# Kernel optimization log

Measured on AMD Instinct MI355X. Metric: run time of the kernel, lower is better.

## Reference

```python
import jax, jax.numpy as jnp
import numpy as np

NUM_EMBEDDINGS = 1024
EMBEDDING_DIM = 64
COMMITMENT_COST = 0.25


def setup_inputs() -> dict:
    key = jax.random.key(0)
    k1, k2 = jax.random.split(key)
    inputs = jax.random.normal(k1, (8, 128, 128, EMBEDDING_DIM), dtype=jnp.float32)
    # nn.Embedding init: uniform(-1/K, 1/K)
    codebook = jax.random.uniform(
        k2, (NUM_EMBEDDINGS, EMBEDDING_DIM), dtype=jnp.float32,
        minval=-1.0 / NUM_EMBEDDINGS, maxval=1.0 / NUM_EMBEDDINGS)
    return {"inputs": inputs, "codebook": codebook}


def reference(inputs, codebook):
    input_shape = inputs.shape
    flat = inputs.reshape(-1, EMBEDDING_DIM)  # [N, D]
    distances = (jnp.sum(flat * flat, axis=1, keepdims=True)
                 + jnp.sum(codebook * codebook, axis=1)
                 - 2.0 * jnp.matmul(flat, codebook.T))  # [N, K]
    encoding_indices = jnp.argmin(distances, axis=1)  # [N]
    # one-hot @ codebook == direct gather
    quantized = codebook[encoding_indices].reshape(input_shape)
    e_latent_loss = jnp.mean((jax.lax.stop_gradient(quantized) - inputs) ** 2)
    q_latent_loss = jnp.mean((quantized - jax.lax.stop_gradient(inputs)) ** 2)
    vq_loss = q_latent_loss + COMMITMENT_COST * e_latent_loss
    # straight-through estimator
    quantized = inputs + jax.lax.stop_gradient(quantized - inputs)
    return (quantized, vq_loss, encoding_indices[:, None])
```

## Files before the change

kernel.cpp:

```cpp
#include <hip/hip_runtime.h>


typedef _Float16 f16x8 __attribute__((ext_vector_type(8)));
typedef float f32x4 __attribute__((ext_vector_type(4)));

constexpr int Dm = 64;
constexpr int Kn = 1024;
constexpr long NR = 131072;
constexpr long QE = NR * (long)Dm;
constexpr int RB = 64;
constexpr int NBLK = (int)(NR / RB);
constexpr int CH = 64;
constexpr int NCH = Kn / CH;
constexpr int SP4 = 17;

constexpr size_t SE_OFF   = 0;
constexpr size_t CBH_OFF  = 4096;
constexpr size_t CNT_OFF  = CBH_OFF + 131072;
constexpr size_t HARD_OFF = CNT_OFF + 256;
constexpr size_t PART_OFF = HARD_OFF + 4 * 131072;
constexpr size_t WS_REQ   = PART_OFF + 16384;

__global__ __launch_bounds__(256) void vq_prep(const float* __restrict__ cb,
                                               float* __restrict__ se,
                                               _Float16* __restrict__ cbh,
                                               int* __restrict__ cnt)
{
    int j = blockIdx.x * 256 + threadIdx.x;
    const float* e = cb + (size_t)j * Dm;
    _Float16* h = cbh + (size_t)j * Dm;
    float s = 0.f;
    #pragma unroll
    for (int d = 0; d < Dm; ++d) s = fmaf(e[d], e[d], s);
    se[j] = s;
    #pragma unroll
    for (int d = 0; d < Dm; ++d) h[d] = (_Float16)(e[d] * 1024.0f);
    if (j == 0) *cnt = 0;
}

__global__ __launch_bounds__(256, 4) void vq_pass1(
    const float* __restrict__ inp, const _Float16* __restrict__ cbh,
    const float* __restrict__ seg, float* __restrict__ out,
    int* __restrict__ hard_list, int* __restrict__ cnt)
{
    __shared__ __align__(16) _Float16 xh[RB * 72];
    __shared__ float se[Kn];
    __shared__ float gs[RB];
    __shared__ float wm1[4][RB], wm2[4][RB];
    __shared__ int   wi1[4][RB];

    const int tid = threadIdx.x;
    const long rbase = (long)blockIdx.x * RB;

    #pragma unroll
    for (int k = 0; k < 4; ++k) se[tid + 256 * k] = seg[tid + 256 * k];

    {
        const int r = tid >> 2, q = tid & 3;
        const float* src = inp + (rbase + r) * Dm + q * 16;
        _Float16* dst = xh + r * 72 + q * 16;
        #pragma unroll
        for (int i = 0; i < 4; ++i) {
            float4 v = *reinterpret_cast<const float4*>(src + 4 * i);
            dst[4*i+0] = (_Float16)v.x; dst[4*i+1] = (_Float16)v.y;
            dst[4*i+2] = (_Float16)v.z; dst[4*i+3] = (_Float16)v.w;
        }
    }
    if (tid < RB) {
        const float* xr = inp + (rbase + tid) * Dm;
        float g = 0.f;
        #pragma unroll
        for (int d = 0; d < Dm; ++d) g += fabsf(xr[d]);
        gs[tid] = g;
    }
    __syncthreads();

    const int w = tid >> 6, l = tid & 63;
    const int arow = l & 15, kg = l >> 4;

    f16x8 a0[4], a1[4];
    #pragma unroll
    for (int rt = 0; rt < 4; ++rt) {
        const _Float16* ap = xh + (rt * 16 + arow) * 72 + kg * 8;
        a0[rt] = *reinterpret_cast<const f16x8*>(ap);
        a1[rt] = *reinterpret_cast<const f16x8*>(ap + 32);
    }

    float mn1[4][4], mn2[4][4]; int ix1[4][4];
    #pragma unroll
    for (int rt = 0; rt < 4; ++rt)
        #pragma unroll
        for (int r = 0; r < 4; ++r) {
            mn1[rt][r] = __builtin_inff(); mn2[rt][r] = __builtin_inff();
            ix1[rt][r] = 0;
        }

    const int code0 = w * 256 + arow;
    const _Float16* bp = cbh + (size_t)code0 * Dm + kg * 8;

    #pragma unroll 2
    for (int t = 0; t < 16; ++t) {
        const _Float16* tp = bp + t * 16 * Dm;
        f16x8 b0 = *reinterpret_cast<const f16x8*>(tp);
        f16x8 b1 = *reinterpret_cast<const f16x8*>(tp + 32);
        const int code = code0 + t * 16;
        const float sec = se[code];
        #pragma unroll
        for (int rt = 0; rt < 4; ++rt) {
            f32x4 acc = {0.f, 0.f, 0.f, 0.f};
            acc = __builtin_amdgcn_mfma_f32_16x16x32_f16(a0[rt], b0, acc, 0, 0, 0);
            acc = __builtin_amdgcn_mfma_f32_16x16x32_f16(a1[rt], b1, acc, 0, 0, 0);
            #pragma unroll
            for (int r = 0; r < 4; ++r) {
                float m = fmaf(acc[r], -0.001953125f, sec);
                mn2[rt][r] = fminf(mn2[rt][r], fmaxf(mn1[rt][r], m));
                ix1[rt][r] = (m < mn1[rt][r]) ? code : ix1[rt][r];
                mn1[rt][r] = fminf(mn1[rt][r], m);
            }
        }
    }

    #pragma unroll
    for (int rt = 0; rt < 4; ++rt)
        #pragma unroll
        for (int r = 0; r < 4; ++r) {
            float m1v = mn1[rt][r], m2v = mn2[rt][r]; int i1v = ix1[rt][r];
            #pragma unroll
            for (int off = 1; off < 16; off <<= 1) {
                float om1 = __shfl_xor(m1v, off);
                float om2 = __shfl_xor(m2v, off);
                int   oi1 = __shfl_xor(i1v, off);
                float nm2 = fminf(fminf(m2v, om2), fmaxf(m1v, om1));
                i1v = (om1 < m1v) ? oi1 : i1v;
                m1v = fminf(m1v, om1);
                m2v = nm2;
            }
            if (arow == 0) {
                const int row = rt * 16 + kg * 4 + r;
                wm1[w][row] = m1v; wm2[w][row] = m2v; wi1[w][row] = i1v;
            }
        }
    __syncthreads();

    if (tid < RB) {
        float m1v = wm1[0][tid], m2v = wm2[0][tid]; int i1v = wi1[0][tid];
        #pragma unroll
        for (int q = 1; q < 4; ++q) {
            float am1 = wm1[q][tid], am2 = wm2[q][tid]; int ai = wi1[q][tid];
            float nm2 = fminf(fminf(m2v, am2), fmaxf(m1v, am1));
            i1v = (am1 < m1v) ? ai : i1v;
            m1v = fminf(m1v, am1);
            m2v = nm2;
        }
        const float T = fmaf(gs[tid], 5.2e-6f, 4.0e-5f);
        const int easy = (m2v - m1v) > T;
        if (easy) out[QE + 1 + rbase + tid] = (float)i1v;
        unsigned long long hm = __ballot(!easy);
        const int nh = __popcll(hm);
        int base = 0;
        if (tid == 0 && nh) base = atomicAdd(cnt, nh);
        base = __shfl(base, 0);
        if (!easy) {
            const int pos = base + __popcll(hm & ((1ull << tid) - 1ull));
            hard_list[pos] = (int)(rbase + tid);
        }
    }
}

__global__ __launch_bounds__(256) void vq_pass2(
    const float* __restrict__ inp, const float* __restrict__ cb,
    const float* __restrict__ seg, float* __restrict__ out,
    const int* __restrict__ hard_list, const int* __restrict__ cnt)
{
    __shared__ float4 xs[RB * SP4];
    __shared__ float4 es[CH * SP4];
    __shared__ float  ses[Kn];
    __shared__ float  sxs[RB];
    __shared__ int    hr[RB];
    __shared__ float  bd[RB * 17];
    __shared__ int    bi[RB * 17];

    const int tid = threadIdx.x;
    const int tr = tid & 15;
    const int tc = tid >> 4;

    #pragma unroll
    for (int k = 0; k < 4; ++k) ses[tid + 256 * k] = seg[tid + 256 * k];

    const int total = *cnt;
    const int nchunk = (total + RB - 1) / RB;
    const float4* gcb = reinterpret_cast<const float4*>(cb);

    for (int c = blockIdx.x; c < nchunk; c += gridDim.x) {
        __syncthreads();
        if (tid < RB) {
            int gi = c * RB + tid;
            hr[tid] = (gi < total) ? hard_list[gi] : -1;
        }
        __syncthreads();

        #pragma unroll
        for (int r = 0; r < 4; ++r) {
            int g = r * 256 + tid;
            int row = g >> 4, col = g & 15;
            int gr = hr[row];
            float4 v = {0.f, 0.f, 0.f, 0.f};
            if (gr >= 0)
                v = *reinterpret_cast<const float4*>(inp + (size_t)gr * Dm + col * 4);
            xs[row * SP4 + col] = v;
        }
        __syncthreads();

        if (tid < RB) {
            const float* xr = reinterpret_cast<const float*>(&xs[tid * SP4]);
            float s = 0.f;
            #pragma unroll
            for (int d = 0; d < Dm; ++d) s = fmaf(xr[d], xr[d], s);
            sxs[tid] = s;
        }
        __syncthreads();

        float sxr[4];
        #pragma unroll
        for (int rr = 0; rr < 4; ++rr) sxr[rr] = sxs[tr + 16 * rr];

        float best[4]; int bidx[4];
        #pragma unroll
        for (int rr = 0; rr < 4; ++rr) { best[rr] = __builtin_inff(); bidx[rr] = 0; }

        for (int ch = 0; ch < NCH; ++ch) {
            __syncthreads();
            #pragma unroll
            for (int r = 0; r < 4; ++r) {
                int g = r * 256 + tid;
                es[(g >> 4) * SP4 + (g & 15)] = gcb[(size_t)ch * (CH * Dm / 4) + g];
            }
            __syncthreads();

            float acc[4][4];
            #pragma unroll
            for (int rr = 0; rr < 4; ++rr)
                #pragma unroll
                for (int cc = 0; cc < 4; ++cc) acc[rr][cc] = 0.f;

            #pragma unroll 4
            for (int db = 0; db < 16; ++db) {
                float4 xf[4], ef[4];
                #pragma unroll
                for (int rr = 0; rr < 4; ++rr) xf[rr] = xs[(tr + 16 * rr) * SP4 + db];
                #pragma unroll
                for (int cc = 0; cc < 4; ++cc) ef[cc] = es[(tc + 16 * cc) * SP4 + db];
                #pragma unroll
                for (int rr = 0; rr < 4; ++rr)
                    #pragma unroll
                    for (int cc = 0; cc < 4; ++cc) {
                        float a = acc[rr][cc];
                        a = fmaf(xf[rr].x, ef[cc].x, a);
                        a = fmaf(xf[rr].y, ef[cc].y, a);
                        a = fmaf(xf[rr].z, ef[cc].z, a);
                        a = fmaf(xf[rr].w, ef[cc].w, a);
                        acc[rr][cc] = a;
                    }
            }

            const int cbase = ch * CH;
            #pragma unroll
            for (int cc = 0; cc < 4; ++cc) {
                const int code = cbase + tc + 16 * cc;
                const float sec = ses[code];
                #pragma unroll
                for (int rr = 0; rr < 4; ++rr) {
                    float dist = (sxr[rr] + sec) - 2.0f * acc[rr][cc];
                    if (dist < best[rr]) { best[rr] = dist; bidx[rr] = code; }
                }
            }
        }

        #pragma unroll
        for (int rr = 0; rr < 4; ++rr) {
            int row = tr + 16 * rr;
            bd[row * 17 + tc] = best[rr];
            bi[row * 17 + tc] = bidx[rr];
        }
        __syncthreads();

        if (tid < RB && hr[tid] >= 0) {
            float b = bd[tid * 17]; int ii = bi[tid * 17];
            #pragma unroll
            for (int q = 1; q < 16; ++q) {
                float d = bd[tid * 17 + q]; int iq = bi[tid * 17 + q];
                if (d < b || (d == b && iq < ii)) { b = d; ii = iq; }
            }
            out[QE + 1 + hr[tid]] = (float)ii;
        }
    }
}

__global__ __launch_bounds__(256) void vq_quant(const float* __restrict__ inp,
                                                const float* __restrict__ cb,
                                                float* __restrict__ out,
                                                double* __restrict__ part)
{
    __shared__ double red[256];
    const int tid = threadIdx.x;
    const long rbase = (long)blockIdx.x * RB;
    const int r2 = tid >> 2;
    const int dq = (tid & 3) * 16;
    const long grow = rbase + r2;

    const int code = (int)out[QE + 1 + grow];
    const float* xr2 = inp + grow * (long)Dm + dq;
    const float* q2  = cb + (size_t)code * Dm + dq;
    float* outq = out + grow * (long)Dm + dq;
    double s = 0.0;
    #pragma unroll
    for (int d0 = 0; d0 < 16; d0 += 4) {
        float4 xv = *reinterpret_cast<const float4*>(xr2 + d0);
        float4 qv = *reinterpret_cast<const float4*>(q2 + d0);
        float4 ov;
        float m0 = qv.x - xv.x; ov.x = xv.x + m0;
        float m1 = qv.y - xv.y; ov.y = xv.y + m1;
        float m2 = qv.z - xv.z; ov.z = xv.z + m2;
        float m3 = qv.w - xv.w; ov.w = xv.w + m3;
        s += (double)m0*m0 + (double)m1*m1 + (double)m2*m2 + (double)m3*m3;
        *reinterpret_cast<float4*>(outq + d0) = ov;
    }

    red[tid] = s;
    __syncthreads();
    for (int k = 128; k > 0; k >>= 1) {
        if (tid < k) red[tid] += red[tid + k];
        __syncthreads();
    }
    if (tid == 0) part[blockIdx.x] = red[0];
}

__global__ __launch_bounds__(256) void vq_fin(const double* __restrict__ part,
                                              float* __restrict__ out)
{
    __shared__ double red[256];
    const int tid = threadIdx.x;
    double s = 0.0;
    #pragma unroll
    for (int k = 0; k < 8; ++k) s += part[tid + 256 * k];
    red[tid] = s;
    __syncthreads();
    for (int k = 128; k > 0; k >>= 1) {
        if (tid < k) red[tid] += red[tid + k];
        __syncthreads();
    }
    if (tid == 0) {
        float m = (float)(red[0] / (double)QE);
        out[QE] = m + 0.25f * m;
    }
}

extern "C" void kernel_launch(void* const* d_in, const int* in_sizes, int n_in,
                              void* d_out, int out_size, void* d_ws, size_t ws_size,
                              hipStream_t stream)
{
    const float* inp = (const float*)d_in[0];
    const float* cb  = (const float*)d_in[1];
    float* out = (float*)d_out;
    char* ws = (char*)d_ws;

    float*    se   = (float*)(ws + SE_OFF);
    _Float16* cbh  = (_Float16*)(ws + CBH_OFF);
    int*      cnt  = (int*)(ws + CNT_OFF);
    int*      hard = (int*)(ws + HARD_OFF);
    double*   part = (double*)(ws + PART_OFF);

    vq_prep<<<4, 256, 0, stream>>>(cb, se, cbh, cnt);
    vq_pass1<<<NBLK, 256, 0, stream>>>(inp, cbh, se, out, hard, cnt);
    vq_pass2<<<512, 256, 0, stream>>>(inp, cb, se, out, hard, cnt);
    vq_quant<<<NBLK, 256, 0, stream>>>(inp, cb, out, part);
    vq_fin<<<1, 256, 0, stream>>>(part, out);
}
```

Measured before the change: 145.7 us.

## Split pass1 work by rows per wave and fuse final loss reduction via atomics

```diff
diff --git a/kernel.cpp b/kernel.cpp
--- a/kernel.cpp
+++ b/kernel.cpp
@@ -18,8 +18,7 @@
 constexpr size_t CBH_OFF  = 4096;
 constexpr size_t CNT_OFF  = CBH_OFF + 131072;
 constexpr size_t HARD_OFF = CNT_OFF + 256;
-constexpr size_t PART_OFF = HARD_OFF + 4 * 131072;
-constexpr size_t WS_REQ   = PART_OFF + 16384;
+constexpr size_t WS_REQ   = HARD_OFF + 4 * 131072 + 256;
 
 __global__ __launch_bounds__(256) void vq_prep(const float* __restrict__ cb,
                                                float* __restrict__ se,
@@ -35,10 +34,14 @@
     se[j] = s;
     #pragma unroll
     for (int d = 0; d < Dm; ++d) h[d] = (_Float16)(e[d] * 1024.0f);
-    if (j == 0) *cnt = 0;
-}
-
-__global__ __launch_bounds__(256, 4) void vq_pass1(
+    if (j == 0) {
+        *cnt = 0;
+        *(unsigned long long*)((char*)cnt + 8) = 0ull;
+        *(unsigned int*)((char*)cnt + 16) = 0u;
+    }
+}
+
+__global__ __launch_bounds__(256, 6) void vq_pass1(
     const float* __restrict__ inp, const _Float16* __restrict__ cbh,
     const float* __restrict__ seg, float* __restrict__ out,
     int* __restrict__ hard_list, int* __restrict__ cnt)
@@ -46,8 +49,8 @@
     __shared__ __align__(16) _Float16 xh[RB * 72];
     __shared__ float se[Kn];
     __shared__ float gs[RB];
-    __shared__ float wm1[4][RB], wm2[4][RB];
-    __shared__ int   wi1[4][RB];
+    __shared__ float fm1[RB], fm2[RB];
+    __shared__ int   fi1[RB];
 
     const int tid = threadIdx.x;
     const long rbase = (long)blockIdx.x * RB;
@@ -76,82 +79,61 @@
     __syncthreads();
 
     const int w = tid >> 6, l = tid & 63;
-    const int arow = l & 15, kg = l >> 4;
-
-    f16x8 a0[4], a1[4];
-    #pragma unroll
-    for (int rt = 0; rt < 4; ++rt) {
-        const _Float16* ap = xh + (rt * 16 + arow) * 72 + kg * 8;
-        a0[rt] = *reinterpret_cast<const f16x8*>(ap);
-        a1[rt] = *reinterpret_cast<const f16x8*>(ap + 32);
-    }
-
-    float mn1[4][4], mn2[4][4]; int ix1[4][4];
-    #pragma unroll
-    for (int rt = 0; rt < 4; ++rt)
-        #pragma unroll
-        for (int r = 0; r < 4; ++r) {
-            mn1[rt][r] = __builtin_inff(); mn2[rt][r] = __builtin_inff();
-            ix1[rt][r] = 0;
-        }
-
-    const int code0 = w * 256 + arow;
-    const _Float16* bp = cbh + (size_t)code0 * Dm + kg * 8;
-
+    const int cl = l & 15, kg = l >> 4;
+
+    const _Float16* ap = xh + (w * 16 + cl) * 72 + kg * 8;
+    const f16x8 a0 = *reinterpret_cast<const f16x8*>(ap);
+    const f16x8 a1 = *reinterpret_cast<const f16x8*>(ap + 32);
+
+    float mn1[4], mn2[4]; int ix1[4];
+    #pragma unroll
+    for (int r = 0; r < 4; ++r) {
+        mn1[r] = __builtin_inff(); mn2[r] = __builtin_inff(); ix1[r] = 0;
+    }
+
+    const _Float16* bp = cbh + (size_t)cl * Dm + kg * 8;
     #pragma unroll 2
-    for (int t = 0; t < 16; ++t) {
+    for (int t = 0; t < 64; ++t) {
         const _Float16* tp = bp + t * 16 * Dm;
         f16x8 b0 = *reinterpret_cast<const f16x8*>(tp);
         f16x8 b1 = *reinterpret_cast<const f16x8*>(tp + 32);
-        const int code = code0 + t * 16;
+        const int code = t * 16 + cl;
         const float sec = se[code];
-        #pragma unroll
-        for (int rt = 0; rt < 4; ++rt) {
-            f32x4 acc = {0.f, 0.f, 0.f, 0.f};
-            acc = __builtin_amdgcn_mfma_f32_16x16x32_f16(a0[rt], b0, acc, 0, 0, 0);
-            acc = __builtin_amdgcn_mfma_f32_16x16x32_f16(a1[rt], b1, acc, 0, 0, 0);
-            #pragma unroll
-            for (int r = 0; r < 4; ++r) {
-                float m = fmaf(acc[r], -0.001953125f, sec);
-                mn2[rt][r] = fminf(mn2[rt][r], fmaxf(mn1[rt][r], m));
-                ix1[rt][r] = (m < mn1[rt][r]) ? code : ix1[rt][r];
-                mn1[rt][r] = fminf(mn1[rt][r], m);
-            }
-        }
-    }
-
-    #pragma unroll
-    for (int rt = 0; rt < 4; ++rt)
+        f32x4 acc = {0.f, 0.f, 0.f, 0.f};
+        acc = __builtin_amdgcn_mfma_f32_16x16x32_f16(a0, b0, acc, 0, 0, 0);
+        acc = __builtin_amdgcn_mfma_f32_16x16x32_f16(a1, b1, acc, 0, 0, 0);
         #pragma unroll
         for (int r = 0; r < 4; ++r) {
-            float m1v = mn1[rt][r], m2v = mn2[rt][r]; int i1v = ix1[rt][r];
-            #pragma unroll
-            for (int off = 1; off < 16; off <<= 1) {
-                float om1 = __shfl_xor(m1v, off);
-                float om2 = __shfl_xor(m2v, off);
-                int   oi1 = __shfl_xor(i1v, off);
-                float nm2 = fminf(fminf(m2v, om2), fmaxf(m1v, om1));
-                i1v = (om1 < m1v) ? oi1 : i1v;
-                m1v = fminf(m1v, om1);
-                m2v = nm2;
-            }
-            if (arow == 0) {
-                const int row = rt * 16 + kg * 4 + r;
-                wm1[w][row] = m1v; wm2[w][row] = m2v; wi1[w][row] = i1v;
-            }
-        }
+            float m = fmaf(acc[r], -0.001953125f, sec);
+            mn2[r] = fminf(mn2[r], fmaxf(mn1[r], m));
+            ix1[r] = (m < mn1[r]) ? code : ix1[r];
+            mn1[r] = fminf(mn1[r], m);
+        }
+    }
+
+    #pragma unroll
+    for (int r = 0; r < 4; ++r) {
+        float m1v = mn1[r], m2v = mn2[r]; int i1v = ix1[r];
+        #pragma unroll
+        for (int off = 1; off < 16; off <<= 1) {
+            float om1 = __shfl_xor(m1v, off);
+            float om2 = __shfl_xor(m2v, off);
+            int   oi1 = __shfl_xor(i1v, off);
+            float nm2 = fminf(fminf(m2v, om2), fmaxf(m1v, om1));
+            i1v = (om1 < m1v) ? oi1 : i1v;
+            m1v = fminf(m1v, om1);
+            m2v = nm2;
+        }
+        if (cl == 0) {
+            const int row = w * 16 + kg * 4 + r;
+            fm1[row] = m1v; fm2[row] = m2v; fi1[row] = i1v;
+        }
+    }
     __syncthreads();
 
     if (tid < RB) {
-        float m1v = wm1[0][tid], m2v = wm2[0][tid]; int i1v = wi1[0][tid];
-        #pragma unroll
-        for (int q = 1; q < 4; ++q) {
-            float am1 = wm1[q][tid], am2 = wm2[q][tid]; int ai = wi1[q][tid];
-            float nm2 = fminf(fminf(m2v, am2), fmaxf(m1v, am1));
-            i1v = (am1 < m1v) ? ai : i1v;
-            m1v = fminf(m1v, am1);
-            m2v = nm2;
-        }
+        const float m1v = fm1[tid], m2v = fm2[tid];
+        const int i1v = fi1[tid];
         const float T = fmaf(gs[tid], 5.2e-6f, 4.0e-5f);
         const int easy = (m2v - m1v) > T;
         if (easy) out[QE + 1 + rbase + tid] = (float)i1v;
@@ -299,7 +281,7 @@
 __global__ __launch_bounds__(256) void vq_quant(const float* __restrict__ inp,
                                                 const float* __restrict__ cb,
                                                 float* __restrict__ out,
-                                                double* __restrict__ part)
+                                                int* __restrict__ cnt)
 {
     __shared__ double red[256];
     const int tid = threadIdx.x;
@@ -332,26 +314,19 @@
         if (tid < k) red[tid] += red[tid + k];
         __syncthreads();
     }
-    if (tid == 0) part[blockIdx.x] = red[0];
-}
-
-__global__ __launch_bounds__(256) void vq_fin(const double* __restrict__ part,
-                                              float* __restrict__ out)
-{
-    __shared__ double red[256];
-    const int tid = threadIdx.x;
-    double s = 0.0;
-    #pragma unroll
-    for (int k = 0; k < 8; ++k) s += part[tid + 256 * k];
-    red[tid] = s;
-    __syncthreads();
-    for (int k = 128; k > 0; k >>= 1) {
-        if (tid < k) red[tid] += red[tid + k];
-        __syncthreads();
-    }
     if (tid == 0) {
-        float m = (float)(red[0] / (double)QE);
-        out[QE] = m + 0.25f * m;
+        unsigned long long* lacc = (unsigned long long*)((char*)cnt + 8);
+        unsigned int* ticket = (unsigned int*)((char*)cnt + 16);
+        unsigned long long f = (unsigned long long)(red[0] * 1048576.0 + 0.5);
+        atomicAdd(lacc, f);
+        __threadfence();
+        unsigned int old = atomicAdd(ticket, 1u);
+        if (old == (unsigned int)(NBLK - 1)) {
+            unsigned long long tot = atomicAdd(lacc, 0ull);
+            double total = (double)tot * (1.0 / 1048576.0);
+            float m = (float)(total / (double)QE);
+            out[QE] = m + 0.25f * m;
+        }
     }
 }
 
@@ -368,11 +343,9 @@
     _Float16* cbh  = (_Float16*)(ws + CBH_OFF);
     int*      cnt  = (int*)(ws + CNT_OFF);
     int*      hard = (int*)(ws + HARD_OFF);
-    double*   part = (double*)(ws + PART_OFF);
 
     vq_prep<<<4, 256, 0, stream>>>(cb, se, cbh, cnt);
     vq_pass1<<<NBLK, 256, 0, stream>>>(inp, cbh, se, out, hard, cnt);
     vq_pass2<<<512, 256, 0, stream>>>(inp, cb, se, out, hard, cnt);
-    vq_quant<<<NBLK, 256, 0, stream>>>(inp, cb, out, part);
-    vq_fin<<<1, 256, 0, stream>>>(part, out);
-}
+    vq_quant<<<NBLK, 256, 0, stream>>>(inp, cb, out, cnt);
+}
```

Result: slower. 301.6 us (+107.0%).

## Fuse quantized output and loss into argmin passes, prefetch codebook fragments

Applied to the files above, without the earlier changes.

```diff
diff --git a/kernel.cpp b/kernel.cpp
--- a/kernel.cpp
+++ b/kernel.cpp
@@ -18,8 +18,9 @@
 constexpr size_t CBH_OFF  = 4096;
 constexpr size_t CNT_OFF  = CBH_OFF + 131072;
 constexpr size_t HARD_OFF = CNT_OFF + 256;
-constexpr size_t PART_OFF = HARD_OFF + 4 * 131072;
-constexpr size_t WS_REQ   = PART_OFF + 16384;
+constexpr size_t RL_OFF   = HARD_OFF + 4 * 131072;
+constexpr size_t PART_OFF = RL_OFF + 4 * 131072;
+constexpr size_t WS_REQ   = PART_OFF + 4096;
 
 __global__ __launch_bounds__(256) void vq_prep(const float* __restrict__ cb,
                                                float* __restrict__ se,
@@ -39,15 +40,19 @@
 }
 
 __global__ __launch_bounds__(256, 4) void vq_pass1(
-    const float* __restrict__ inp, const _Float16* __restrict__ cbh,
-    const float* __restrict__ seg, float* __restrict__ out,
-    int* __restrict__ hard_list, int* __restrict__ cnt)
+    const float* __restrict__ inp, const float* __restrict__ cb,
+    const _Float16* __restrict__ cbh, const float* __restrict__ seg,
+    float* __restrict__ out, int* __restrict__ hard_list, int* __restrict__ cnt,
+    float* __restrict__ row_loss)
 {
     __shared__ __align__(16) _Float16 xh[RB * 72];
     __shared__ float se[Kn];
     __shared__ float gs[RB];
     __shared__ float wm1[4][RB], wm2[4][RB];
     __shared__ int   wi1[4][RB];
+    __shared__ int   ridx[RB];
+    __shared__ int   easyf[RB];
+    __shared__ double qd[RB][4];
 
     const int tid = threadIdx.x;
     const long rbase = (long)blockIdx.x * RB;
@@ -98,18 +103,21 @@
     const int code0 = w * 256 + arow;
     const _Float16* bp = cbh + (size_t)code0 * Dm + kg * 8;
 
+    f16x8 b0 = *reinterpret_cast<const f16x8*>(bp);
+    f16x8 b1 = *reinterpret_cast<const f16x8*>(bp + 32);
     #pragma unroll 2
     for (int t = 0; t < 16; ++t) {
-        const _Float16* tp = bp + t * 16 * Dm;
-        f16x8 b0 = *reinterpret_cast<const f16x8*>(tp);
-        f16x8 b1 = *reinterpret_cast<const f16x8*>(tp + 32);
+        f16x8 c0 = b0, c1 = b1;
+        const _Float16* tpn = bp + ((t + 1) & 15) * 16 * Dm;
+        b0 = *reinterpret_cast<const f16x8*>(tpn);
+        b1 = *reinterpret_cast<const f16x8*>(tpn + 32);
         const int code = code0 + t * 16;
         const float sec = se[code];
         #pragma unroll
         for (int rt = 0; rt < 4; ++rt) {
             f32x4 acc = {0.f, 0.f, 0.f, 0.f};
-            acc = __builtin_amdgcn_mfma_f32_16x16x32_f16(a0[rt], b0, acc, 0, 0, 0);
-            acc = __builtin_amdgcn_mfma_f32_16x16x32_f16(a1[rt], b1, acc, 0, 0, 0);
+            acc = __builtin_amdgcn_mfma_f32_16x16x32_f16(a0[rt], c0, acc, 0, 0, 0);
+            acc = __builtin_amdgcn_mfma_f32_16x16x32_f16(a1[rt], c1, acc, 0, 0, 0);
             #pragma unroll
             for (int r = 0; r < 4; ++r) {
                 float m = fmaf(acc[r], -0.001953125f, sec);
@@ -154,6 +162,8 @@
         }
         const float T = fmaf(gs[tid], 5.2e-6f, 4.0e-5f);
         const int easy = (m2v - m1v) > T;
+        ridx[tid] = i1v;
+        easyf[tid] = easy;
         if (easy) out[QE + 1 + rbase + tid] = (float)i1v;
         unsigned long long hm = __ballot(!easy);
         const int nh = __popcll(hm);
@@ -165,12 +175,42 @@
             hard_list[pos] = (int)(rbase + tid);
         }
     }
+    __syncthreads();
+
+    const int r2 = tid >> 2;
+    const int dq = (tid & 3) * 16;
+    if (easyf[r2]) {
+        const long grow = rbase + r2;
+        const float* xr2 = inp + grow * (long)Dm + dq;
+        const float* q2  = cb + (size_t)ridx[r2] * Dm + dq;
+        float* outq = out + grow * (long)Dm + dq;
+        double s = 0.0;
+        #pragma unroll
+        for (int d0 = 0; d0 < 16; d0 += 4) {
+            float4 xv = *reinterpret_cast<const float4*>(xr2 + d0);
+            float4 qv = *reinterpret_cast<const float4*>(q2 + d0);
+            float4 ov;
+            float m0 = qv.x - xv.x; ov.x = xv.x + m0;
+            float m1 = qv.y - xv.y; ov.y = xv.y + m1;
+            float m2 = qv.z - xv.z; ov.z = xv.z + m2;
+            float m3 = qv.w - xv.w; ov.w = xv.w + m3;
+            s += (double)m0*m0 + (double)m1*m1 + (double)m2*m2 + (double)m3*m3;
+            *reinterpret_cast<float4*>(outq + d0) = ov;
+        }
+        qd[r2][tid & 3] = s;
+    }
+    __syncthreads();
+    if (tid < RB && easyf[tid]) {
+        double s = qd[tid][0] + qd[tid][1] + qd[tid][2] + qd[tid][3];
+        row_loss[rbase + tid] = (float)s;
+    }
 }
 
 __global__ __launch_bounds__(256) void vq_pass2(
     const float* __restrict__ inp, const float* __restrict__ cb,
     const float* __restrict__ seg, float* __restrict__ out,
-    const int* __restrict__ hard_list, const int* __restrict__ cnt)
+    const int* __restrict__ hard_list, const int* __restrict__ cnt,
+    float* __restrict__ row_loss)
 {
     __shared__ float4 xs[RB * SP4];
     __shared__ float4 es[CH * SP4];
@@ -179,6 +219,8 @@
     __shared__ int    hr[RB];
     __shared__ float  bd[RB * 17];
     __shared__ int    bi[RB * 17];
+    __shared__ int    comb[RB];
+    __shared__ double qd[RB][4];
 
     const int tid = threadIdx.x;
     const int tr = tid & 15;
@@ -291,42 +333,47 @@
                 float d = bd[tid * 17 + q]; int iq = bi[tid * 17 + q];
                 if (d < b || (d == b && iq < ii)) { b = d; ii = iq; }
             }
+            comb[tid] = ii;
             out[QE + 1 + hr[tid]] = (float)ii;
         }
-    }
-}
-
-__global__ __launch_bounds__(256) void vq_quant(const float* __restrict__ inp,
-                                                const float* __restrict__ cb,
-                                                float* __restrict__ out,
-                                                double* __restrict__ part)
+        __syncthreads();
+
+        const int r2 = tid >> 2;
+        const int dq = (tid & 3) * 16;
+        if (hr[r2] >= 0) {
+            const long grow = hr[r2];
+            const float* xr2 = inp + grow * (long)Dm + dq;
+            const float* q2  = cb + (size_t)comb[r2] * Dm + dq;
+            float* outq = out + grow * (long)Dm + dq;
+            double s = 0.0;
+            #pragma unroll
+            for (int d0 = 0; d0 < 16; d0 += 4) {
+                float4 xv = *reinterpret_cast<const float4*>(xr2 + d0);
+                float4 qv = *reinterpret_cast<const float4*>(q2 + d0);
+                float4 ov;
+                float m0 = qv.x - xv.x; ov.x = xv.x + m0;
+                float m1 = qv.y - xv.y; ov.y = xv.y + m1;
+                float m2 = qv.z - xv.z; ov.z = xv.z + m2;
+                float m3 = qv.w - xv.w; ov.w = xv.w + m3;
+                s += (double)m0*m0 + (double)m1*m1 + (double)m2*m2 + (double)m3*m3;
+                *reinterpret_cast<float4*>(outq + d0) = ov;
+            }
+            qd[r2][tid & 3] = s;
+        }
+        __syncthreads();
+        if (tid < RB && hr[tid] >= 0) {
+            double s = qd[tid][0] + qd[tid][1] + qd[tid][2] + qd[tid][3];
+            row_loss[hr[tid]] = (float)s;
+        }
+    }
+}
+
+__global__ __launch_bounds__(256) void vq_lred(const float* __restrict__ row_loss,
+                                               double* __restrict__ part)
 {
     __shared__ double red[256];
     const int tid = threadIdx.x;
-    const long rbase = (long)blockIdx.x * RB;
-    const int r2 = tid >> 2;
-    const int dq = (tid & 3) * 16;
-    const long grow = rbase + r2;
-
-    const int code = (int)out[QE + 1 + grow];
-    const float* xr2 = inp + grow * (long)Dm + dq;
-    const float* q2  = cb + (size_t)code * Dm + dq;
-    float* outq = out + grow * (long)Dm + dq;
-    double s = 0.0;
-    #pragma unroll
-    for (int d0 = 0; d0 < 16; d0 += 4) {
-        float4 xv = *reinterpret_cast<const float4*>(xr2 + d0);
-        float4 qv = *reinterpret_cast<const float4*>(q2 + d0);
-        float4 ov;
-        float m0 = qv.x - xv.x; ov.x = xv.x + m0;
-        float m1 = qv.y - xv.y; ov.y = xv.y + m1;
-        float m2 = qv.z - xv.z; ov.z = xv.z + m2;
-        float m3 = qv.w - xv.w; ov.w = xv.w + m3;
-        s += (double)m0*m0 + (double)m1*m1 + (double)m2*m2 + (double)m3*m3;
-        *reinterpret_cast<float4*>(outq + d0) = ov;
-    }
-
-    red[tid] = s;
+    red[tid] = (double)row_loss[(size_t)blockIdx.x * 256 + tid];
     __syncthreads();
     for (int k = 128; k > 0; k >>= 1) {
         if (tid < k) red[tid] += red[tid + k];
@@ -340,10 +387,7 @@
 {
     __shared__ double red[256];
     const int tid = threadIdx.x;
-    double s = 0.0;
-    #pragma unroll
-    for (int k = 0; k < 8; ++k) s += part[tid + 256 * k];
-    red[tid] = s;
+    red[tid] = part[tid] + part[tid + 256];
     __syncthreads();
     for (int k = 128; k > 0; k >>= 1) {
         if (tid < k) red[tid] += red[tid + k];
@@ -368,11 +412,12 @@
     _Float16* cbh  = (_Float16*)(ws + CBH_OFF);
     int*      cnt  = (int*)(ws + CNT_OFF);
     int*      hard = (int*)(ws + HARD_OFF);
+    float*    rl   = (float*)(ws + RL_OFF);
     double*   part = (double*)(ws + PART_OFF);
 
     vq_prep<<<4, 256, 0, stream>>>(cb, se, cbh, cnt);
-    vq_pass1<<<NBLK, 256, 0, stream>>>(inp, cbh, se, out, hard, cnt);
-    vq_pass2<<<512, 256, 0, stream>>>(inp, cb, se, out, hard, cnt);
-    vq_quant<<<NBLK, 256, 0, stream>>>(inp, cb, out, part);
+    vq_pass1<<<NBLK, 256, 0, stream>>>(inp, cb, cbh, se, out, hard, cnt, rl);
+    vq_pass2<<<512, 256, 0, stream>>>(inp, cb, se, out, hard, cnt, rl);
+    vq_lred<<<512, 256, 0, stream>>>(rl, part);
     vq_fin<<<1, 256, 0, stream>>>(part, out);
 }
```

Result: faster. 141.5 us (-2.9%).
